# Kernel optimization log

Measured on AMD Instinct MI355X. Metric: run time of the kernel, lower is better.

The kernel has to match this reference:

```python
import jax, jax.numpy as jnp
import numpy as np

D_MODEL = 1024
H = 16
D_HEAD = D_MODEL // H


def setup_inputs() -> dict:
    key = jax.random.key(0)
    ks = jax.random.split(key, 9)
    B, S = 2, 2048
    x = jax.random.normal(ks[0], (B, S, D_MODEL), dtype=jnp.float32)
    s = 1.0 / np.sqrt(D_HEAD)
    # per-head Q/K/V linears, stacked: W[h, out, in], b[h, out] (torch Linear: y = x W^T + b)
    Wq = jax.random.normal(ks[1], (H, D_HEAD, D_HEAD), dtype=jnp.float32) * s
    bq = jax.random.normal(ks[2], (H, D_HEAD), dtype=jnp.float32) * 0.01
    Wk = jax.random.normal(ks[3], (H, D_HEAD, D_HEAD), dtype=jnp.float32) * s
    bk = jax.random.normal(ks[4], (H, D_HEAD), dtype=jnp.float32) * 0.01
    Wv = jax.random.normal(ks[5], (H, D_HEAD, D_HEAD), dtype=jnp.float32) * s
    bv = jax.random.normal(ks[6], (H, D_HEAD), dtype=jnp.float32) * 0.01
    Wo = jax.random.normal(ks[7], (D_MODEL, D_MODEL), dtype=jnp.float32) / np.sqrt(D_MODEL)
    bo = jax.random.normal(ks[8], (D_MODEL,), dtype=jnp.float32) * 0.01
    return {"x": x, "Wq": Wq, "bq": bq, "Wk": Wk, "bk": bk,
            "Wv": Wv, "bv": bv, "Wo": Wo, "bo": bo}


def reference(x, Wq, bq, Wk, bk, Wv, bv, Wo, bo):
    B, S, D = x.shape
    xh = x.reshape(B, S, H, D_HEAD)  # split along feature dim, head-major
    q = jnp.einsum('bshi,hoi->bsho', xh, Wq) + bq
    k = jnp.einsum('bshi,hoi->bsho', xh, Wk) + bk
    v = jnp.einsum('bshi,hoi->bsho', xh, Wv) + bv
    scale = 1.0 / jnp.sqrt(jnp.asarray(D_HEAD, dtype=x.dtype))  # source scales by sqrt(d_model//h)
    scores = jnp.einsum('bqhd,bkhd->bhqk', q, k) * scale
    causal = jnp.tril(jnp.ones((S, S), dtype=bool))
    scores = jnp.where(causal, scores, -jnp.inf)
    attn = jax.nn.softmax(scores, axis=-1)
    out = jnp.einsum('bhqk,bkhd->bqhd', attn, v).reshape(B, S, D)
    return out @ Wo.T + bo
```

## Files before the change

kernel.cpp:

```cpp
#include <hip/hip_runtime.h>
#include <cstddef>

#define Bc 2
#define Sc 2048
#define Dc 1024
#define Hc 16
#define QSC 0.18033688011112042f

typedef short short8 __attribute__((ext_vector_type(8)));
typedef float floatx4 __attribute__((ext_vector_type(4)));
typedef unsigned short ushort_t;

#if __has_builtin(__builtin_amdgcn_exp2f)
#define EXP2F(x) __builtin_amdgcn_exp2f(x)
#else
#define EXP2F(x) exp2f(x)
#endif

__device__ __forceinline__ unsigned pack2bf(float a, float b) {
    unsigned ua = __float_as_uint(a) + 0x8000u;
    unsigned ub = __float_as_uint(b) + 0x8000u;
    return __builtin_amdgcn_perm(ub, ua, 0x07060302u);
}
__device__ __forceinline__ ushort_t f2bf(float f) {
    return (ushort_t)((__float_as_uint(f) + 0x8000u) >> 16);
}

__global__ __launch_bounds__(256) void wcvt_kernel(
    const float* __restrict__ Wo, const float* __restrict__ Wq,
    const float* __restrict__ Wk, const float* __restrict__ Wv,
    ushort_t* __restrict__ WoB, ushort_t* __restrict__ Wqkvb)
{
    int idx = (blockIdx.x * 256 + threadIdx.x) * 8;
    const float* src; ushort_t* dst;
    if (idx < 1048576) { src = Wo + idx; dst = WoB + idx; }
    else {
        int r = idx - 1048576;
        int w = r >> 16, off = r & 65535;
        src = (w == 0 ? Wq : (w == 1 ? Wk : Wv)) + off;
        dst = Wqkvb + r;
    }
    float4 a = *(const float4*)src;
    float4 c = *(const float4*)(src + 4);
    uint4 o;
    o.x = pack2bf(a.x, a.y); o.y = pack2bf(a.z, a.w);
    o.z = pack2bf(c.x, c.y); o.w = pack2bf(c.z, c.w);
    *(uint4*)dst = o;
}

__global__ __launch_bounds__(256) void qkv_kernel(
    const float* __restrict__ x, const ushort_t* __restrict__ Wqkvb,
    const float* __restrict__ bq, const float* __restrict__ bk, const float* __restrict__ bv,
    ushort_t* __restrict__ Qb, ushort_t* __restrict__ Kb, ushort_t* __restrict__ VT)
{
    const int blk = blockIdx.x;
    const int st = blk & 31, h = (blk >> 5) & 15, b = blk >> 9;
    const int bh = b * Hc + h, s0 = st * 64;
    const int tid = threadIdx.x, wid = tid >> 6, lane = tid & 63;
    const int lr = lane & 15, quad = lane >> 4;

    __shared__ ushort_t Xs[64 * 72];
    __shared__ ushort_t Wsh[3 * 64 * 72];

    {
        int row = tid >> 2, cg = tid & 3;
        const float* xp = x + ((size_t)(b * Sc + s0 + row)) * Dc + h * 64 + cg * 16;
        float4 v0 = *(const float4*)xp;
        float4 v1 = *(const float4*)(xp + 4);
        float4 v2 = *(const float4*)(xp + 8);
        float4 v3 = *(const float4*)(xp + 12);
        uint4 p0, p1;
        p0.x = pack2bf(v0.x, v0.y); p0.y = pack2bf(v0.z, v0.w);
        p0.z = pack2bf(v1.x, v1.y); p0.w = pack2bf(v1.z, v1.w);
        p1.x = pack2bf(v2.x, v2.y); p1.y = pack2bf(v2.z, v2.w);
        p1.z = pack2bf(v3.x, v3.y); p1.w = pack2bf(v3.z, v3.w);
        *(uint4*)(Xs + row * 72 + cg * 16) = p0;
        *(uint4*)(Xs + row * 72 + cg * 16 + 8) = p1;
    }
    {
        const ushort_t* Wg = Wqkvb + (size_t)h * 4096;
#pragma unroll
        for (int s = 0; s < 6; ++s) {
            int c = tid + s * 256;
            int w = c >> 9, rem = c & 511, row = rem >> 3, part = rem & 7;
            *(short8*)(Wsh + (w * 64 + row) * 72 + part * 8) =
                *(const short8*)(Wg + (size_t)w * 65536 + row * 64 + part * 8);
        }
    }
    __syncthreads();

    short8 af0 = *(const short8*)(Xs + (wid * 16 + lr) * 72 + quad * 8);
    short8 af1 = *(const short8*)(Xs + (wid * 16 + lr) * 72 + 32 + quad * 8);

    const float* bias3[3] = {bq + h * 64, bk + h * 64, bv + h * 64};
    const int row = tid >> 2, cg = tid & 3;

#pragma unroll
    for (int w = 0; w < 3; ++w) {
        ushort_t* Ot = Wsh + w * 64 * 72;
        short8 bf0[4], bf1[4];
#pragma unroll
        for (int n = 0; n < 4; ++n) {
            const ushort_t* wrow = Ot + (n * 16 + lr) * 72;
            bf0[n] = *(const short8*)(wrow + quad * 8);
            bf1[n] = *(const short8*)(wrow + 32 + quad * 8);
        }
        floatx4 acc[4];
#pragma unroll
        for (int n = 0; n < 4; ++n) {
            floatx4 z = {0.f, 0.f, 0.f, 0.f};
            acc[n] = __builtin_amdgcn_mfma_f32_16x16x32_bf16(af0, bf0[n], z, 0, 0, 0);
            acc[n] = __builtin_amdgcn_mfma_f32_16x16x32_bf16(af1, bf1[n], acc[n], 0, 0, 0);
        }
        __syncthreads();
        if (w < 2) {
#pragma unroll
            for (int n = 0; n < 4; ++n) {
                float bias = bias3[w][n * 16 + lr];
#pragma unroll
                for (int r = 0; r < 4; ++r) {
                    float val = acc[n][r] + bias;
                    if (w == 0) val *= QSC;
                    Ot[(wid * 16 + quad * 4 + r) * 72 + n * 16 + lr] = f2bf(val);
                }
            }
        } else {
#pragma unroll
            for (int n = 0; n < 4; ++n) {
                float bias = bias3[2][n * 16 + lr];
                uint2 pw;
                pw.x = pack2bf(acc[n][0] + bias, acc[n][1] + bias);
                pw.y = pack2bf(acc[n][2] + bias, acc[n][3] + bias);
                *(uint2*)(Ot + (n * 16 + lr) * 72 + wid * 16 + quad * 4) = pw;
            }
        }
        __syncthreads();
        const ushort_t* srcp = Ot + row * 72 + cg * 16;
        uint4 d0 = *(const uint4*)srcp;
        uint4 d1 = *(const uint4*)(srcp + 8);
        ushort_t* dst;
        if (w == 0)      dst = Qb + ((size_t)bh * Sc + s0 + row) * 64 + cg * 16;
        else if (w == 1) dst = Kb + ((size_t)bh * Sc + s0 + row) * 64 + cg * 16;
        else             dst = VT + ((size_t)bh * 64 + row) * Sc + s0 + cg * 16;
        *(uint4*)dst = d0;
        *(uint4*)(dst + 8) = d1;
    }
}

#define ST 72

__global__ __launch_bounds__(256, 2) void attn_kernel(
    const ushort_t* __restrict__ Qg, const ushort_t* __restrict__ Kg,
    const ushort_t* __restrict__ VTg, ushort_t* __restrict__ Actx)
{
    const int blk = blockIdx.x;
    const int u = blk & 255;
    const int bh = u & 31;
    const int f = (u >> 5) & 7;
    const int tpair = (blk < 256) ? f : 15 - f;
    const int b = bh >> 4, h = bh & 15;
    const int qta = 31 - tpair, qtb = tpair;
    const int s0a = qta * 64, s0b = qtb * 64;
    const int tid = threadIdx.x, wid = tid >> 6, lane = tid & 63;
    const int lr = lane & 15, quad = lane >> 4;

    __shared__ ushort_t Ks[2][64 * ST];
    __shared__ ushort_t Vs[2][64 * ST];

    const ushort_t* Kbh = Kg + (size_t)bh * Sc * 64;
    const ushort_t* Vbh = VTg + (size_t)bh * 64 * Sc;

    const ushort_t* QrA = Qg + ((size_t)bh * Sc + s0a + wid * 16 + lr) * 64;
    const ushort_t* QrB = Qg + ((size_t)bh * Sc + s0b + wid * 16 + lr) * 64;
    short8 qfa0 = *(const short8*)(QrA + quad * 8);
    short8 qfa1 = *(const short8*)(QrA + 32 + quad * 8);
    short8 qfb0 = *(const short8*)(QrB + quad * 8);
    short8 qfb1 = *(const short8*)(QrB + 32 + quad * 8);

    floatx4 oA[4], oB[4];
    float lA = 0.f, lB = 0.f;
#pragma unroll
    for (int n = 0; n < 4; ++n) { oA[n] = floatx4{0,0,0,0}; oB[n] = floatx4{0,0,0,0}; }

    const int sr0 = tid >> 3, sp0 = tid & 7;
    const int sr1 = sr0 + 32;

    short8 kr0 = *(const short8*)(Kbh + (size_t)sr0 * 64 + sp0 * 8);
    short8 kr1 = *(const short8*)(Kbh + (size_t)sr1 * 64 + sp0 * 8);
    short8 vr0 = *(const short8*)(Vbh + (size_t)sr0 * Sc + sp0 * 8);
    short8 vr1 = *(const short8*)(Vbh + (size_t)sr1 * Sc + sp0 * 8);
    *(short8*)(Ks[0] + sr0 * ST + sp0 * 8) = kr0;
    *(short8*)(Ks[0] + sr1 * ST + sp0 * 8) = kr1;
    *(short8*)(Vs[0] + sr0 * ST + sp0 * 8) = vr0;
    *(short8*)(Vs[0] + sr1 * ST + sp0 * 8) = vr1;
    __syncthreads();

    int buf = 0;
    for (int kt = 0; kt <= qta; ++kt) {
        const bool hasB = (kt <= qtb);
        const ushort_t* Kc = Ks[buf];
        const ushort_t* Vc = Vs[buf];

        short8 kf[4][2], vf[4][2];
#pragma unroll
        for (int kg = 0; kg < 4; ++kg) {
            const ushort_t* kp = Kc + (4 * lr + kg) * ST;
            kf[kg][0] = *(const short8*)(kp + quad * 8);
            kf[kg][1] = *(const short8*)(kp + 32 + quad * 8);
        }
#pragma unroll
        for (int n = 0; n < 4; ++n) {
            const ushort_t* vp = Vc + (n * 16 + lr) * ST;
            vf[n][0] = *(const short8*)(vp + 16 * quad);
            vf[n][1] = *(const short8*)(vp + 16 * quad + 8);
        }

        if (kt < qta) {
            const ushort_t* kn = Kbh + (size_t)(kt + 1) * 4096;
            const ushort_t* vn = Vbh + (kt + 1) * 64;
            kr0 = *(const short8*)(kn + (size_t)sr0 * 64 + sp0 * 8);
            kr1 = *(const short8*)(kn + (size_t)sr1 * 64 + sp0 * 8);
            vr0 = *(const short8*)(vn + (size_t)sr0 * Sc + sp0 * 8);
            vr1 = *(const short8*)(vn + (size_t)sr1 * Sc + sp0 * 8);
        }

        floatx4 sA[4], sB[4];
#pragma unroll
        for (int kg = 0; kg < 4; ++kg) {
            floatx4 z = {0.f, 0.f, 0.f, 0.f};
            floatx4 t0 = __builtin_amdgcn_mfma_f32_16x16x32_bf16(kf[kg][0], qfa0, z, 0, 0, 0);
            sA[kg] = __builtin_amdgcn_mfma_f32_16x16x32_bf16(kf[kg][1], qfa1, t0, 0, 0, 0);
        }
        if (hasB) {
#pragma unroll
            for (int kg = 0; kg < 4; ++kg) {
                floatx4 z = {0.f, 0.f, 0.f, 0.f};
                floatx4 t0 = __builtin_amdgcn_mfma_f32_16x16x32_bf16(kf[kg][0], qfb0, z, 0, 0, 0);
                sB[kg] = __builtin_amdgcn_mfma_f32_16x16x32_bf16(kf[kg][1], qfb1, t0, 0, 0, 0);
            }
        }

        const int qrow = wid * 16 + lr;
        if (kt == qta) {
#pragma unroll
            for (int kg = 0; kg < 4; ++kg)
#pragma unroll
                for (int r = 0; r < 4; ++r)
                    if (16 * quad + 4 * r + kg > qrow) sA[kg][r] = -1e30f;
        }
        if (hasB && kt == qtb) {
#pragma unroll
            for (int kg = 0; kg < 4; ++kg)
#pragma unroll
                for (int r = 0; r < 4; ++r)
                    if (16 * quad + 4 * r + kg > qrow) sB[kg][r] = -1e30f;
        }

        {
            float e[4][4];
#pragma unroll
            for (int kg = 0; kg < 4; ++kg)
#pragma unroll
                for (int r = 0; r < 4; ++r) e[kg][r] = EXP2F(sA[kg][r]);
#pragma unroll
            for (int kg = 0; kg < 4; ++kg)
                lA += (e[kg][0] + e[kg][1]) + (e[kg][2] + e[kg][3]);
            union { uint4 u; short8 s; } p0, p1;
            p0.u.x = pack2bf(e[0][0], e[1][0]); p0.u.y = pack2bf(e[2][0], e[3][0]);
            p0.u.z = pack2bf(e[0][1], e[1][1]); p0.u.w = pack2bf(e[2][1], e[3][1]);
            p1.u.x = pack2bf(e[0][2], e[1][2]); p1.u.y = pack2bf(e[2][2], e[3][2]);
            p1.u.z = pack2bf(e[0][3], e[1][3]); p1.u.w = pack2bf(e[2][3], e[3][3]);
#pragma unroll
            for (int n = 0; n < 4; ++n) {
                oA[n] = __builtin_amdgcn_mfma_f32_16x16x32_bf16(p0.s, vf[n][0], oA[n], 0, 0, 0);
                oA[n] = __builtin_amdgcn_mfma_f32_16x16x32_bf16(p1.s, vf[n][1], oA[n], 0, 0, 0);
            }
        }
        if (hasB) {
            float e[4][4];
#pragma unroll
            for (int kg = 0; kg < 4; ++kg)
#pragma unroll
                for (int r = 0; r < 4; ++r) e[kg][r] = EXP2F(sB[kg][r]);
#pragma unroll
            for (int kg = 0; kg < 4; ++kg)
                lB += (e[kg][0] + e[kg][1]) + (e[kg][2] + e[kg][3]);
            union { uint4 u; short8 s; } p0, p1;
            p0.u.x = pack2bf(e[0][0], e[1][0]); p0.u.y = pack2bf(e[2][0], e[3][0]);
            p0.u.z = pack2bf(e[0][1], e[1][1]); p0.u.w = pack2bf(e[2][1], e[3][1]);
            p1.u.x = pack2bf(e[0][2], e[1][2]); p1.u.y = pack2bf(e[2][2], e[3][2]);
            p1.u.z = pack2bf(e[0][3], e[1][3]); p1.u.w = pack2bf(e[2][3], e[3][3]);
#pragma unroll
            for (int n = 0; n < 4; ++n) {
                oB[n] = __builtin_amdgcn_mfma_f32_16x16x32_bf16(p0.s, vf[n][0], oB[n], 0, 0, 0);
                oB[n] = __builtin_amdgcn_mfma_f32_16x16x32_bf16(p1.s, vf[n][1], oB[n], 0, 0, 0);
            }
        }

        if (kt < qta) {
            *(short8*)(Ks[buf ^ 1] + sr0 * ST + sp0 * 8) = kr0;
            *(short8*)(Ks[buf ^ 1] + sr1 * ST + sp0 * 8) = kr1;
            *(short8*)(Vs[buf ^ 1] + sr0 * ST + sp0 * 8) = vr0;
            *(short8*)(Vs[buf ^ 1] + sr1 * ST + sp0 * 8) = vr1;
            buf ^= 1;
        }
        __syncthreads();
    }

    lA += __shfl_xor(lA, 16, 64); lA += __shfl_xor(lA, 32, 64);
    lB += __shfl_xor(lB, 16, 64); lB += __shfl_xor(lB, 32, 64);
    float invA = 1.f / lA, invB = 1.f / lB;
#pragma unroll
    for (int r = 0; r < 4; ++r) {
        float iA = __shfl(invA, 4 * quad + r, 64);
        float iB = __shfl(invB, 4 * quad + r, 64);
        int rowA = s0a + wid * 16 + quad * 4 + r;
        int rowB = s0b + wid * 16 + quad * 4 + r;
        ushort_t* dA = Actx + ((size_t)(b * Sc + rowA)) * Dc + h * 64 + lr;
        ushort_t* dB = Actx + ((size_t)(b * Sc + rowB)) * Dc + h * 64 + lr;
#pragma unroll
        for (int n = 0; n < 4; ++n) {
            dA[n * 16] = f2bf(oA[n][r] * iA);
            dB[n * 16] = f2bf(oB[n][r] * iB);
        }
    }
}

__global__ __launch_bounds__(256, 2) void proj_kernel(
    const ushort_t* __restrict__ Ab, const ushort_t* __restrict__ Wb,
    const float* __restrict__ bo, float* __restrict__ out)
{
    const int bn = blockIdx.x & 15, bm = blockIdx.x >> 4;
    const int tid = threadIdx.x, wid = tid >> 6, lane = tid & 63;
    const int lr = lane & 15, quad = lane >> 4;
    const int wm = wid * 32;

    __shared__ ushort_t As[128 * 40];
    __shared__ ushort_t Bs[64 * 40];

    floatx4 acc[2][4];
#pragma unroll
    for (int i = 0; i < 2; ++i)
#pragma unroll
        for (int n = 0; n < 4; ++n) acc[i][n] = floatx4{0.f, 0.f, 0.f, 0.f};

    const ushort_t* Ag = Ab + (size_t)bm * 128 * 1024;
    const ushort_t* Wg = Wb + (size_t)bn * 64 * 1024;

    const int ar0 = tid >> 2, ap0 = tid & 3;
    const int ar1 = ar0 + 64;

    short8 a0 = *(const short8*)(Ag + (size_t)ar0 * 1024 + ap0 * 8);
    short8 a1 = *(const short8*)(Ag + (size_t)ar1 * 1024 + ap0 * 8);
    short8 b0 = *(const short8*)(Wg + (size_t)ar0 * 1024 + ap0 * 8);
    *(short8*)(As + ar0 * 40 + ap0 * 8) = a0;
    *(short8*)(As + ar1 * 40 + ap0 * 8) = a1;
    *(short8*)(Bs + ar0 * 40 + ap0 * 8) = b0;
    __syncthreads();

    for (int k0 = 0; k0 < 1024; k0 += 32) {
        short8 fa0 = *(const short8*)(As + (wm + lr) * 40 + quad * 8);
        short8 fa1 = *(const short8*)(As + (wm + 16 + lr) * 40 + quad * 8);
        short8 fb[4];
#pragma unroll
        for (int n = 0; n < 4; ++n)
            fb[n] = *(const short8*)(Bs + (n * 16 + lr) * 40 + quad * 8);

        if (k0 < 992) {
            int k1 = k0 + 32;
            a0 = *(const short8*)(Ag + (size_t)ar0 * 1024 + k1 + ap0 * 8);
            a1 = *(const short8*)(Ag + (size_t)ar1 * 1024 + k1 + ap0 * 8);
            b0 = *(const short8*)(Wg + (size_t)ar0 * 1024 + k1 + ap0 * 8);
        }
#pragma unroll
        for (int n = 0; n < 4; ++n) {
            acc[0][n] = __builtin_amdgcn_mfma_f32_16x16x32_bf16(fa0, fb[n], acc[0][n], 0, 0, 0);
            acc[1][n] = __builtin_amdgcn_mfma_f32_16x16x32_bf16(fa1, fb[n], acc[1][n], 0, 0, 0);
        }
        __syncthreads();
        if (k0 < 992) {
            *(short8*)(As + ar0 * 40 + ap0 * 8) = a0;
            *(short8*)(As + ar1 * 40 + ap0 * 8) = a1;
            *(short8*)(Bs + ar0 * 40 + ap0 * 8) = b0;
            __syncthreads();
        }
    }

#pragma unroll
    for (int i = 0; i < 2; ++i) {
        int mrow = bm * 128 + wm + i * 16 + quad * 4;
#pragma unroll
        for (int n = 0; n < 4; ++n) {
            int col = bn * 64 + n * 16 + lr;
            float bias = bo[col];
#pragma unroll
            for (int r = 0; r < 4; ++r)
                out[(size_t)(mrow + r) * 1024 + col] = acc[i][n][r] + bias;
        }
    }
}

extern "C" void kernel_launch(void* const* d_in, const int* in_sizes, int n_in,
                              void* d_out, int out_size, void* d_ws, size_t ws_size,
                              hipStream_t stream)
{
    (void)in_sizes; (void)n_in; (void)out_size; (void)ws_size;
    const float* x  = (const float*)d_in[0];
    const float* Wq = (const float*)d_in[1];
    const float* bq = (const float*)d_in[2];
    const float* Wk = (const float*)d_in[3];
    const float* bk = (const float*)d_in[4];
    const float* Wv = (const float*)d_in[5];
    const float* bv = (const float*)d_in[6];
    const float* Wo = (const float*)d_in[7];
    const float* bo = (const float*)d_in[8];
    float* out = (float*)d_out;

    const size_t N4 = (size_t)Bc * Hc * Sc * 64;
    ushort_t* base  = (ushort_t*)d_ws;
    ushort_t* Qb    = base;
    ushort_t* Kb    = base + N4;
    ushort_t* VT    = base + 2 * N4;
    ushort_t* Actx  = base + 3 * N4;
    ushort_t* WoB   = base + 4 * N4;
    ushort_t* Wqkvb = base + 4 * N4 + 1048576;

    wcvt_kernel<<<dim3(608), dim3(256), 0, stream>>>(Wo, Wq, Wk, Wv, WoB, Wqkvb);
    qkv_kernel<<<dim3(Bc * Hc * (Sc / 64)), dim3(256), 0, stream>>>(
        x, Wqkvb, bq, bk, bv, Qb, Kb, VT);
    attn_kernel<<<dim3(512), dim3(256), 0, stream>>>(Qb, Kb, VT, Actx);
    proj_kernel<<<dim3(32 * 16), dim3(256), 0, stream>>>(Actx, WoB, bo, out);
}
```

Measured before the change: 143.5 us.

## Use direct global-to-LDS loads with pre-swizzled K/V tiles in attention and projection

The QKV kernel now writes K and V as contiguous 64x64 tiles with an XOR swizzle baked in, so the attention kernel can stream each tile into LDS with global_load_lds DMA instead of staging through registers. The projection GEMM also switches to double-buffered LDS filled by global_load_lds, dropping the padded layout and the second barrier per iteration. The goal is to free registers and VALU/LDS-store work and to overlap the next tile's fetch with the MFMA work. In exchange it relies on the unpadded proj LDS layout, which may cause bank conflicts, and on the async DMA being correctly fenced by the existing barriers.

```diff
diff --git a/kernel.cpp b/kernel.cpp
--- a/kernel.cpp
+++ b/kernel.cpp
@@ -24,6 +24,13 @@
 }
 __device__ __forceinline__ ushort_t f2bf(float f) {
     return (ushort_t)((__float_as_uint(f) + 0x8000u) >> 16);
+}
+
+__device__ __forceinline__ void dma16(const void* g, void* l) {
+    __builtin_amdgcn_global_load_lds(
+        (const __attribute__((address_space(1))) unsigned int*)g,
+        (__attribute__((address_space(3))) unsigned int*)l,
+        16, 0, 0);
 }
 
 __global__ __launch_bounds__(256) void wcvt_kernel(
@@ -51,7 +58,7 @@
 __global__ __launch_bounds__(256) void qkv_kernel(
     const float* __restrict__ x, const ushort_t* __restrict__ Wqkvb,
     const float* __restrict__ bq, const float* __restrict__ bk, const float* __restrict__ bv,
-    ushort_t* __restrict__ Qb, ushort_t* __restrict__ Kb, ushort_t* __restrict__ VT)
+    ushort_t* __restrict__ Qb, ushort_t* __restrict__ Kt, ushort_t* __restrict__ Vt)
 {
     const int blk = blockIdx.x;
     const int st = blk & 31, h = (blk >> 5) & 15, b = blk >> 9;
@@ -138,20 +145,23 @@
         const ushort_t* srcp = Ot + row * 72 + cg * 16;
         uint4 d0 = *(const uint4*)srcp;
         uint4 d1 = *(const uint4*)(srcp + 8);
-        ushort_t* dst;
-        if (w == 0)      dst = Qb + ((size_t)bh * Sc + s0 + row) * 64 + cg * 16;
-        else if (w == 1) dst = Kb + ((size_t)bh * Sc + s0 + row) * 64 + cg * 16;
-        else             dst = VT + ((size_t)bh * 64 + row) * Sc + s0 + cg * 16;
-        *(uint4*)dst = d0;
-        *(uint4*)(dst + 8) = d1;
-    }
-}
-
-#define ST 72
+        if (w == 0) {
+            ushort_t* dst = Qb + ((size_t)bh * Sc + s0 + row) * 64 + cg * 16;
+            *(uint4*)dst = d0;
+            *(uint4*)(dst + 8) = d1;
+        } else {
+            ushort_t* tile = (w == 1 ? Kt : Vt) + ((size_t)(bh * 32 + st)) * 4096;
+            char* rb = (char*)(tile + row * 64);
+            int sw = (row & 7) << 4;
+            *(uint4*)(rb + ((cg * 32) ^ sw)) = d0;
+            *(uint4*)(rb + ((cg * 32 + 16) ^ sw)) = d1;
+        }
+    }
+}
 
 __global__ __launch_bounds__(256, 2) void attn_kernel(
-    const ushort_t* __restrict__ Qg, const ushort_t* __restrict__ Kg,
-    const ushort_t* __restrict__ VTg, ushort_t* __restrict__ Actx)
+    const ushort_t* __restrict__ Qg, const ushort_t* __restrict__ Ktg,
+    const ushort_t* __restrict__ Vtg, ushort_t* __restrict__ Actx)
 {
     const int blk = blockIdx.x;
     const int u = blk & 255;
@@ -164,11 +174,11 @@
     const int tid = threadIdx.x, wid = tid >> 6, lane = tid & 63;
     const int lr = lane & 15, quad = lane >> 4;
 
-    __shared__ ushort_t Ks[2][64 * ST];
-    __shared__ ushort_t Vs[2][64 * ST];
-
-    const ushort_t* Kbh = Kg + (size_t)bh * Sc * 64;
-    const ushort_t* Vbh = VTg + (size_t)bh * 64 * Sc;
+    __shared__ ushort_t Ks[2][64 * 64];
+    __shared__ ushort_t Vs[2][64 * 64];
+
+    const char* KbhB = (const char*)(Ktg + (size_t)bh * 32 * 4096);
+    const char* VbhB = (const char*)(Vtg + (size_t)bh * 32 * 4096);
 
     const ushort_t* QrA = Qg + ((size_t)bh * Sc + s0a + wid * 16 + lr) * 64;
     const ushort_t* QrB = Qg + ((size_t)bh * Sc + s0b + wid * 16 + lr) * 64;
@@ -182,46 +192,48 @@
 #pragma unroll
     for (int n = 0; n < 4; ++n) { oA[n] = floatx4{0,0,0,0}; oB[n] = floatx4{0,0,0,0}; }
 
-    const int sr0 = tid >> 3, sp0 = tid & 7;
-    const int sr1 = sr0 + 32;
-
-    short8 kr0 = *(const short8*)(Kbh + (size_t)sr0 * 64 + sp0 * 8);
-    short8 kr1 = *(const short8*)(Kbh + (size_t)sr1 * 64 + sp0 * 8);
-    short8 vr0 = *(const short8*)(Vbh + (size_t)sr0 * Sc + sp0 * 8);
-    short8 vr1 = *(const short8*)(Vbh + (size_t)sr1 * Sc + sp0 * 8);
-    *(short8*)(Ks[0] + sr0 * ST + sp0 * 8) = kr0;
-    *(short8*)(Ks[0] + sr1 * ST + sp0 * 8) = kr1;
-    *(short8*)(Vs[0] + sr0 * ST + sp0 * 8) = vr0;
-    *(short8*)(Vs[0] + sr1 * ST + sp0 * 8) = vr1;
+    const int doff = wid * 2048 + lane * 16;
+
+    dma16(KbhB + doff,        (char*)Ks[0] + doff);
+    dma16(KbhB + doff + 1024, (char*)Ks[0] + doff + 1024);
+    dma16(VbhB + doff,        (char*)Vs[0] + doff);
+    dma16(VbhB + doff + 1024, (char*)Vs[0] + doff + 1024);
     __syncthreads();
 
     int buf = 0;
     for (int kt = 0; kt <= qta; ++kt) {
         const bool hasB = (kt <= qtb);
-        const ushort_t* Kc = Ks[buf];
-        const ushort_t* Vc = Vs[buf];
+
+        if (kt < qta) {
+            const char* kn = KbhB + (size_t)(kt + 1) * 8192;
+            const char* vn = VbhB + (size_t)(kt + 1) * 8192;
+            char* kd = (char*)Ks[buf ^ 1];
+            char* vd = (char*)Vs[buf ^ 1];
+            dma16(kn + doff,        kd + doff);
+            dma16(kn + doff + 1024, kd + doff + 1024);
+            dma16(vn + doff,        vd + doff);
+            dma16(vn + doff + 1024, vd + doff + 1024);
+        }
+
+        const char* KcB = (const char*)Ks[buf];
+        const char* VcB = (const char*)Vs[buf];
 
         short8 kf[4][2], vf[4][2];
 #pragma unroll
         for (int kg = 0; kg < 4; ++kg) {
-            const ushort_t* kp = Kc + (4 * lr + kg) * ST;
-            kf[kg][0] = *(const short8*)(kp + quad * 8);
-            kf[kg][1] = *(const short8*)(kp + 32 + quad * 8);
-        }
-#pragma unroll
-        for (int n = 0; n < 4; ++n) {
-            const ushort_t* vp = Vc + (n * 16 + lr) * ST;
-            vf[n][0] = *(const short8*)(vp + 16 * quad);
-            vf[n][1] = *(const short8*)(vp + 16 * quad + 8);
-        }
-
-        if (kt < qta) {
-            const ushort_t* kn = Kbh + (size_t)(kt + 1) * 4096;
-            const ushort_t* vn = Vbh + (kt + 1) * 64;
-            kr0 = *(const short8*)(kn + (size_t)sr0 * 64 + sp0 * 8);
-            kr1 = *(const short8*)(kn + (size_t)sr1 * 64 + sp0 * 8);
-            vr0 = *(const short8*)(vn + (size_t)sr0 * Sc + sp0 * 8);
-            vr1 = *(const short8*)(vn + (size_t)sr1 * Sc + sp0 * 8);
+            int row = 4 * lr + kg;
+            const char* rb = KcB + row * 128;
+            int sw = (row & 7) << 4;
+            kf[kg][0] = *(const short8*)(rb + ((quad * 16) ^ sw));
+            kf[kg][1] = *(const short8*)(rb + ((64 + quad * 16) ^ sw));
+        }
+#pragma unroll
+        for (int n = 0; n < 4; ++n) {
+            int row = n * 16 + lr;
+            const char* rb = VcB + row * 128;
+            int sw = (lr & 7) << 4;
+            vf[n][0] = *(const short8*)(rb + ((quad * 32) ^ sw));
+            vf[n][1] = *(const short8*)(rb + ((quad * 32 + 16) ^ sw));
         }
 
         floatx4 sA[4], sB[4];
@@ -297,14 +309,8 @@
             }
         }
 
-        if (kt < qta) {
-            *(short8*)(Ks[buf ^ 1] + sr0 * ST + sp0 * 8) = kr0;
-            *(short8*)(Ks[buf ^ 1] + sr1 * ST + sp0 * 8) = kr1;
-            *(short8*)(Vs[buf ^ 1] + sr0 * ST + sp0 * 8) = vr0;
-            *(short8*)(Vs[buf ^ 1] + sr1 * ST + sp0 * 8) = vr1;
-            buf ^= 1;
-        }
         __syncthreads();
+        buf ^= 1;
     }
 
     lA += __shfl_xor(lA, 16, 64); lA += __shfl_xor(lA, 32, 64);
@@ -335,8 +341,8 @@
     const int lr = lane & 15, quad = lane >> 4;
     const int wm = wid * 32;
 
-    __shared__ ushort_t As[128 * 40];
-    __shared__ ushort_t Bs[64 * 40];
+    __shared__ ushort_t As[2][128 * 32];
+    __shared__ ushort_t Bs[2][64 * 32];
 
     floatx4 acc[2][4];
 #pragma unroll
@@ -344,46 +350,44 @@
 #pragma unroll
         for (int n = 0; n < 4; ++n) acc[i][n] = floatx4{0.f, 0.f, 0.f, 0.f};
 
-    const ushort_t* Ag = Ab + (size_t)bm * 128 * 1024;
-    const ushort_t* Wg = Wb + (size_t)bn * 64 * 1024;
-
-    const int ar0 = tid >> 2, ap0 = tid & 3;
-    const int ar1 = ar0 + 64;
-
-    short8 a0 = *(const short8*)(Ag + (size_t)ar0 * 1024 + ap0 * 8);
-    short8 a1 = *(const short8*)(Ag + (size_t)ar1 * 1024 + ap0 * 8);
-    short8 b0 = *(const short8*)(Wg + (size_t)ar0 * 1024 + ap0 * 8);
-    *(short8*)(As + ar0 * 40 + ap0 * 8) = a0;
-    *(short8*)(As + ar1 * 40 + ap0 * 8) = a1;
-    *(short8*)(Bs + ar0 * 40 + ap0 * 8) = b0;
+    const char* AgB = (const char*)(Ab + (size_t)bm * 128 * 1024);
+    const char* WgB = (const char*)(Wb + (size_t)bn * 64 * 1024);
+
+    const int oa = wid * 2048 + lane * 16;
+    const int ob = wid * 1024 + lane * 16;
+    const int ra0 = oa >> 6, ca0 = oa & 63;
+    const int ra1 = (oa + 1024) >> 6, ca1 = (oa + 1024) & 63;
+    const int rb0 = ob >> 6, cb0 = ob & 63;
+
+    dma16(AgB + (size_t)ra0 * 2048 + ca0, (char*)As[0] + oa);
+    dma16(AgB + (size_t)ra1 * 2048 + ca1, (char*)As[0] + oa + 1024);
+    dma16(WgB + (size_t)rb0 * 2048 + cb0, (char*)Bs[0] + ob);
     __syncthreads();
 
+    int buf = 0;
     for (int k0 = 0; k0 < 1024; k0 += 32) {
-        short8 fa0 = *(const short8*)(As + (wm + lr) * 40 + quad * 8);
-        short8 fa1 = *(const short8*)(As + (wm + 16 + lr) * 40 + quad * 8);
+        if (k0 < 992) {
+            int kb = (k0 + 32) * 2;
+            dma16(AgB + (size_t)ra0 * 2048 + kb + ca0, (char*)As[buf ^ 1] + oa);
+            dma16(AgB + (size_t)ra1 * 2048 + kb + ca1, (char*)As[buf ^ 1] + oa + 1024);
+            dma16(WgB + (size_t)rb0 * 2048 + kb + cb0, (char*)Bs[buf ^ 1] + ob);
+        }
+        const ushort_t* Ac = As[buf];
+        const ushort_t* Bcb = Bs[buf];
+        short8 fa0 = *(const short8*)(Ac + (wm + lr) * 32 + quad * 8);
+        short8 fa1 = *(const short8*)(Ac + (wm + 16 + lr) * 32 + quad * 8);
         short8 fb[4];
 #pragma unroll
         for (int n = 0; n < 4; ++n)
-            fb[n] = *(const short8*)(Bs + (n * 16 + lr) * 40 + quad * 8);
-
-        if (k0 < 992) {
-            int k1 = k0 + 32;
-            a0 = *(const short8*)(Ag + (size_t)ar0 * 1024 + k1 + ap0 * 8);
-            a1 = *(const short8*)(Ag + (size_t)ar1 * 1024 + k1 + ap0 * 8);
-            b0 = *(const short8*)(Wg + (size_t)ar0 * 1024 + k1 + ap0 * 8);
-        }
+            fb[n] = *(const short8*)(Bcb + (n * 16 + lr) * 32 + quad * 8);
+
 #pragma unroll
         for (int n = 0; n < 4; ++n) {
             acc[0][n] = __builtin_amdgcn_mfma_f32_16x16x32_bf16(fa0, fb[n], acc[0][n], 0, 0, 0);
             acc[1][n] = __builtin_amdgcn_mfma_f32_16x16x32_bf16(fa1, fb[n], acc[1][n], 0, 0, 0);
         }
         __syncthreads();
-        if (k0 < 992) {
-            *(short8*)(As + ar0 * 40 + ap0 * 8) = a0;
-            *(short8*)(As + ar1 * 40 + ap0 * 8) = a1;
-            *(short8*)(Bs + ar0 * 40 + ap0 * 8) = b0;
-            __syncthreads();
-        }
+        buf ^= 1;
     }
 
 #pragma unroll
@@ -419,15 +423,15 @@
     const size_t N4 = (size_t)Bc * Hc * Sc * 64;
     ushort_t* base  = (ushort_t*)d_ws;
     ushort_t* Qb    = base;
-    ushort_t* Kb    = base + N4;
-    ushort_t* VT    = base + 2 * N4;
+    ushort_t* Kt    = base + N4;
+    ushort_t* Vt    = base + 2 * N4;
     ushort_t* Actx  = base + 3 * N4;
     ushort_t* WoB   = base + 4 * N4;
     ushort_t* Wqkvb = base + 4 * N4 + 1048576;
 
     wcvt_kernel<<<dim3(608), dim3(256), 0, stream>>>(Wo, Wq, Wk, Wv, WoB, Wqkvb);
     qkv_kernel<<<dim3(Bc * Hc * (Sc / 64)), dim3(256), 0, stream>>>(
-        x, Wqkvb, bq, bk, bv, Qb, Kb, VT);
-    attn_kernel<<<dim3(512), dim3(256), 0, stream>>>(Qb, Kb, VT, Actx);
+        x, Wqkvb, bq, bk, bv, Qb, Kt, Vt);
+    attn_kernel<<<dim3(512), dim3(256), 0, stream>>>(Qb, Kt, Vt, Actx);
     proj_kernel<<<dim3(32 * 16), dim3(256), 0, stream>>>(Actx, WoB, bo, out);
 }
```

New measurement: 149.9 us. 1.04x slower.

## Pre-swizzle K/V into MFMA fragment layout and load directly from global

Applied to the files above, without the earlier changes.

The QKV kernel now writes K and V tiles in a per-lane MFMA fragment order, so the attention kernel can load its fragments straight from global memory with coalesced 16-byte loads. This removes the LDS double buffer, the staging stores and the per-iteration __syncthreads. Occupancy is raised to 3 blocks per CU and the block-to-(head, tile) mapping changes. The trade-off is that every wave now loads K/V from global/L2 itself, with no LDS sharing across the four waves and no explicit prefetch, so the loop may become latency-bound.

```diff
diff --git a/kernel.cpp b/kernel.cpp
--- a/kernel.cpp
+++ b/kernel.cpp
@@ -51,7 +51,7 @@
 __global__ __launch_bounds__(256) void qkv_kernel(
     const float* __restrict__ x, const ushort_t* __restrict__ Wqkvb,
     const float* __restrict__ bq, const float* __restrict__ bk, const float* __restrict__ bv,
-    ushort_t* __restrict__ Qb, ushort_t* __restrict__ Kb, ushort_t* __restrict__ VT)
+    ushort_t* __restrict__ Qb, ushort_t* __restrict__ Kf, ushort_t* __restrict__ Vf)
 {
     const int blk = blockIdx.x;
     const int st = blk & 31, h = (blk >> 5) & 15, b = blk >> 9;
@@ -135,40 +135,45 @@
             }
         }
         __syncthreads();
-        const ushort_t* srcp = Ot + row * 72 + cg * 16;
-        uint4 d0 = *(const uint4*)srcp;
-        uint4 d1 = *(const uint4*)(srcp + 8);
-        ushort_t* dst;
-        if (w == 0)      dst = Qb + ((size_t)bh * Sc + s0 + row) * 64 + cg * 16;
-        else if (w == 1) dst = Kb + ((size_t)bh * Sc + s0 + row) * 64 + cg * 16;
-        else             dst = VT + ((size_t)bh * 64 + row) * Sc + s0 + cg * 16;
-        *(uint4*)dst = d0;
-        *(uint4*)(dst + 8) = d1;
-    }
-}
-
-#define ST 72
-
-__global__ __launch_bounds__(256, 2) void attn_kernel(
-    const ushort_t* __restrict__ Qg, const ushort_t* __restrict__ Kg,
-    const ushort_t* __restrict__ VTg, ushort_t* __restrict__ Actx)
+        if (w == 0) {
+            const ushort_t* srcp = Ot + row * 72 + cg * 16;
+            uint4 d0 = *(const uint4*)srcp;
+            uint4 d1 = *(const uint4*)(srcp + 8);
+            ushort_t* dst = Qb + ((size_t)bh * Sc + s0 + row) * 64 + cg * 16;
+            *(uint4*)dst = d0;
+            *(uint4*)(dst + 8) = d1;
+        } else if (w == 1) {
+            uint4 d0 = *(const uint4*)(Ot + (4 * lr + wid) * 72 + 8 * quad);
+            uint4 d1 = *(const uint4*)(Ot + (4 * lr + wid) * 72 + 32 + 8 * quad);
+            ushort_t* dstb = Kf + ((size_t)(bh * 32 + st)) * 4096 + wid * 1024 + lane * 8;
+            *(uint4*)dstb = d0;
+            *(uint4*)(dstb + 512) = d1;
+        } else {
+            uint4 d0 = *(const uint4*)(Ot + (wid * 16 + lr) * 72 + 16 * quad);
+            uint4 d1 = *(const uint4*)(Ot + (wid * 16 + lr) * 72 + 16 * quad + 8);
+            ushort_t* dstb = Vf + ((size_t)(bh * 32 + st)) * 4096 + wid * 1024 + lane * 8;
+            *(uint4*)dstb = d0;
+            *(uint4*)(dstb + 512) = d1;
+        }
+    }
+}
+
+__global__ __launch_bounds__(256, 3) void attn_kernel(
+    const ushort_t* __restrict__ Qg, const ushort_t* __restrict__ Kfg,
+    const ushort_t* __restrict__ Vfg, ushort_t* __restrict__ Actx)
 {
     const int blk = blockIdx.x;
-    const int u = blk & 255;
-    const int bh = u & 31;
-    const int f = (u >> 5) & 7;
-    const int tpair = (blk < 256) ? f : 15 - f;
+    const int x = blk & 7, u = blk >> 3;
+    const int bh = (u & 3) * 8 + x;
+    const int f = u >> 2;
     const int b = bh >> 4, h = bh & 15;
-    const int qta = 31 - tpair, qtb = tpair;
+    const int qta = 31 - f, qtb = f;
     const int s0a = qta * 64, s0b = qtb * 64;
     const int tid = threadIdx.x, wid = tid >> 6, lane = tid & 63;
     const int lr = lane & 15, quad = lane >> 4;
 
-    __shared__ ushort_t Ks[2][64 * ST];
-    __shared__ ushort_t Vs[2][64 * ST];
-
-    const ushort_t* Kbh = Kg + (size_t)bh * Sc * 64;
-    const ushort_t* Vbh = VTg + (size_t)bh * 64 * Sc;
+    const ushort_t* Kfb = Kfg + (size_t)bh * 32 * 4096 + lane * 8;
+    const ushort_t* Vfb = Vfg + (size_t)bh * 32 * 4096 + lane * 8;
 
     const ushort_t* QrA = Qg + ((size_t)bh * Sc + s0a + wid * 16 + lr) * 64;
     const ushort_t* QrB = Qg + ((size_t)bh * Sc + s0b + wid * 16 + lr) * 64;
@@ -182,46 +187,21 @@
 #pragma unroll
     for (int n = 0; n < 4; ++n) { oA[n] = floatx4{0,0,0,0}; oB[n] = floatx4{0,0,0,0}; }
 
-    const int sr0 = tid >> 3, sp0 = tid & 7;
-    const int sr1 = sr0 + 32;
-
-    short8 kr0 = *(const short8*)(Kbh + (size_t)sr0 * 64 + sp0 * 8);
-    short8 kr1 = *(const short8*)(Kbh + (size_t)sr1 * 64 + sp0 * 8);
-    short8 vr0 = *(const short8*)(Vbh + (size_t)sr0 * Sc + sp0 * 8);
-    short8 vr1 = *(const short8*)(Vbh + (size_t)sr1 * Sc + sp0 * 8);
-    *(short8*)(Ks[0] + sr0 * ST + sp0 * 8) = kr0;
-    *(short8*)(Ks[0] + sr1 * ST + sp0 * 8) = kr1;
-    *(short8*)(Vs[0] + sr0 * ST + sp0 * 8) = vr0;
-    *(short8*)(Vs[0] + sr1 * ST + sp0 * 8) = vr1;
-    __syncthreads();
-
-    int buf = 0;
     for (int kt = 0; kt <= qta; ++kt) {
         const bool hasB = (kt <= qtb);
-        const ushort_t* Kc = Ks[buf];
-        const ushort_t* Vc = Vs[buf];
+        const ushort_t* Kt = Kfb + (size_t)kt * 4096;
+        const ushort_t* Vt = Vfb + (size_t)kt * 4096;
 
         short8 kf[4][2], vf[4][2];
 #pragma unroll
         for (int kg = 0; kg < 4; ++kg) {
-            const ushort_t* kp = Kc + (4 * lr + kg) * ST;
-            kf[kg][0] = *(const short8*)(kp + quad * 8);
-            kf[kg][1] = *(const short8*)(kp + 32 + quad * 8);
-        }
-#pragma unroll
-        for (int n = 0; n < 4; ++n) {
-            const ushort_t* vp = Vc + (n * 16 + lr) * ST;
-            vf[n][0] = *(const short8*)(vp + 16 * quad);
-            vf[n][1] = *(const short8*)(vp + 16 * quad + 8);
-        }
-
-        if (kt < qta) {
-            const ushort_t* kn = Kbh + (size_t)(kt + 1) * 4096;
-            const ushort_t* vn = Vbh + (kt + 1) * 64;
-            kr0 = *(const short8*)(kn + (size_t)sr0 * 64 + sp0 * 8);
-            kr1 = *(const short8*)(kn + (size_t)sr1 * 64 + sp0 * 8);
-            vr0 = *(const short8*)(vn + (size_t)sr0 * Sc + sp0 * 8);
-            vr1 = *(const short8*)(vn + (size_t)sr1 * Sc + sp0 * 8);
+            kf[kg][0] = *(const short8*)(Kt + kg * 1024);
+            kf[kg][1] = *(const short8*)(Kt + kg * 1024 + 512);
+        }
+#pragma unroll
+        for (int n = 0; n < 4; ++n) {
+            vf[n][0] = *(const short8*)(Vt + n * 1024);
+            vf[n][1] = *(const short8*)(Vt + n * 1024 + 512);
         }
 
         floatx4 sA[4], sB[4];
@@ -296,15 +276,6 @@
                 oB[n] = __builtin_amdgcn_mfma_f32_16x16x32_bf16(p1.s, vf[n][1], oB[n], 0, 0, 0);
             }
         }
-
-        if (kt < qta) {
-            *(short8*)(Ks[buf ^ 1] + sr0 * ST + sp0 * 8) = kr0;
-            *(short8*)(Ks[buf ^ 1] + sr1 * ST + sp0 * 8) = kr1;
-            *(short8*)(Vs[buf ^ 1] + sr0 * ST + sp0 * 8) = vr0;
-            *(short8*)(Vs[buf ^ 1] + sr1 * ST + sp0 * 8) = vr1;
-            buf ^= 1;
-        }
-        __syncthreads();
     }
 
     lA += __shfl_xor(lA, 16, 64); lA += __shfl_xor(lA, 32, 64);
@@ -419,15 +390,15 @@
     const size_t N4 = (size_t)Bc * Hc * Sc * 64;
     ushort_t* base  = (ushort_t*)d_ws;
     ushort_t* Qb    = base;
-    ushort_t* Kb    = base + N4;
-    ushort_t* VT    = base + 2 * N4;
+    ushort_t* Kf    = base + N4;
+    ushort_t* Vf    = base + 2 * N4;
     ushort_t* Actx  = base + 3 * N4;
     ushort_t* WoB   = base + 4 * N4;
     ushort_t* Wqkvb = base + 4 * N4 + 1048576;
 
     wcvt_kernel<<<dim3(608), dim3(256), 0, stream>>>(Wo, Wq, Wk, Wv, WoB, Wqkvb);
     qkv_kernel<<<dim3(Bc * Hc * (Sc / 64)), dim3(256), 0, stream>>>(
-        x, Wqkvb, bq, bk, bv, Qb, Kb, VT);
-    attn_kernel<<<dim3(512), dim3(256), 0, stream>>>(Qb, Kb, VT, Actx);
+        x, Wqkvb, bq, bk, bv, Qb, Kf, Vf);
+    attn_kernel<<<dim3(512), dim3(256), 0, stream>>>(Qb, Kf, Vf, Actx);
     proj_kernel<<<dim3(32 * 16), dim3(256), 0, stream>>>(Actx, WoB, bo, out);
 }
```

Result: no change. 142.0 us (-1.0%).
